# Kernel tuning notes

Hardware: AMD Instinct MI355X
Metric: run time of the kernel (lower is better)

Reference implementation:

```python
import jax, jax.numpy as jnp
import numpy as np

WINDOW = (2, 8, 8)  # (T, H, W); N = 128
NUM_HEADS = 6
DIM = 192


def _relative_position_index(ws):
    """NxN int index into the relative-position-bias table (faithful port)."""
    d, h, w = np.meshgrid(np.arange(ws[0]), np.arange(ws[1]), np.arange(ws[2]), indexing='ij')
    coords = np.stack([d, h, w]).reshape(3, -1)            # (3, N)
    rel = coords[:, :, None] - coords[:, None, :]          # (3, N, N)
    rel = rel.transpose(1, 2, 0).astype(np.int64)          # (N, N, 3)
    rel[:, :, 0] += ws[0] - 1
    rel[:, :, 1] += ws[1] - 1
    rel[:, :, 2] += ws[2] - 1
    rel[:, :, 0] *= (2 * ws[1] - 1) * (2 * ws[2] - 1)
    rel[:, :, 1] *= 2 * ws[2] - 1
    return rel.sum(-1)                                     # (N, N)


def setup_inputs() -> dict:
    key = jax.random.key(0)
    k1, k2, k3, k4, k5, k6 = jax.random.split(key, 6)
    N = WINDOW[0] * WINDOW[1] * WINDOW[2]                  # 128
    B_ = 1024                                              # num_windows * batch
    nW = 64
    table_len = (2 * WINDOW[0] - 1) * (2 * WINDOW[1] - 1) * (2 * WINDOW[2] - 1)  # 675
    x = jax.random.normal(k1, (B_, N, DIM), dtype=jnp.float32)
    mask = jax.random.normal(k2, (nW, N, N), dtype=jnp.float32)  # additive attn mask
    qkv_w = jax.random.normal(k3, (3 * DIM, DIM), dtype=jnp.float32) * 0.02
    proj_w = jax.random.normal(k4, (DIM, DIM), dtype=jnp.float32) * 0.02
    proj_b = jax.random.normal(k5, (DIM,), dtype=jnp.float32) * 0.02
    rpb_table = jax.random.normal(k6, (table_len, NUM_HEADS), dtype=jnp.float32) * 0.02
    rel_index = jnp.asarray(_relative_position_index(WINDOW), dtype=jnp.int32)
    return {"x": x, "mask": mask, "qkv_w": qkv_w, "proj_w": proj_w,
            "proj_b": proj_b, "rpb_table": rpb_table, "rel_index": rel_index}


def reference(x, mask, qkv_w, proj_w, proj_b, rpb_table, rel_index):
    B_, N, C = x.shape
    H = NUM_HEADS
    hd = C // H
    scale = hd ** (-0.5)
    # qkv projection (no bias, qkv_bias=False)
    qkv = (x @ qkv_w.T).reshape(B_, N, 3, H, hd)
    q, k, v = qkv[:, :, 0], qkv[:, :, 1], qkv[:, :, 2]      # (B_, N, H, hd)
    # windowed attention scores
    attn = jnp.einsum('bnhd,bmhd->bhnm', q * scale, k)      # (B_, H, N, N)
    # gathered relative-position bias: (N, N, H) -> (H, N, N)
    bias = rpb_table[rel_index.reshape(-1)].reshape(N, N, H).transpose(2, 0, 1)
    attn = attn + bias[None]
    # shift-window mask: (nW, N, N) broadcast over batch groups and heads
    nW = mask.shape[0]
    attn = attn.reshape(B_ // nW, nW, H, N, N) + mask[None, :, None]
    attn = attn.reshape(B_, H, N, N)
    attn = jax.nn.softmax(attn, axis=-1)
    out = jnp.einsum('bhnm,bmhd->bnhd', attn, v).reshape(B_, N, C)
    return out @ proj_w.T + proj_b
```

## Files before the change

### kernel.cpp

```cpp
#include <hip/hip_runtime.h>
#include <hip/hip_bf16.h>


typedef float f32x4 __attribute__((ext_vector_type(4)));
typedef short short8 __attribute__((ext_vector_type(8)));
typedef short short4e __attribute__((ext_vector_type(4)));

#define SCALE 0.17677669529663687f
#define LOG2E 1.4426950408889634f

static __device__ __forceinline__ short f2bf(float f) {
  __hip_bfloat16 h = __float2bfloat16(f);
  return __builtin_bit_cast(short, h);
}
static __device__ __forceinline__ f32x4 mfma16(short8 a, short8 b, f32x4 c) {
  return __builtin_amdgcn_mfma_f32_16x16x32_bf16(a, b, c, 0, 0, 0);
}

__global__ __launch_bounds__(256) void prep_w(const float* __restrict__ qkvw,
                                              const float* __restrict__ projw,
                                              short* __restrict__ wbf,
                                              short* __restrict__ pwbf) {
  int t = blockIdx.x * 256 + threadIdx.x;
  const int NQ = 27648;
  float4 f; short* dst;
  if (t < NQ) { f = ((const float4*)qkvw)[t]; dst = wbf + t * 4; }
  else        { f = ((const float4*)projw)[t - NQ]; dst = pwbf + (t - NQ) * 4; }
  short4e o; o[0] = f2bf(f.x); o[1] = f2bf(f.y); o[2] = f2bf(f.z); o[3] = f2bf(f.w);
  *(short4e*)dst = o;
}

__global__ __launch_bounds__(256) void prep_bias(const int* __restrict__ rel,
                                                 const float* __restrict__ table,
                                                 float* __restrict__ biasF) {
  int blk = blockIdx.x;
  int h = blk >> 4, L = blk & 15;
  int tid = threadIdx.x, lane = tid & 63, wave = tid >> 6;
  int lr = lane & 15, r4 = (lane >> 4) * 4;
  int rf = L >> 3, rg = (L >> 1) & 3, cp = L & 1;
  int row = wave * 32 + rf * 16 + r4 + rg;
  float4 v;
#pragma unroll
  for (int e = 0; e < 4; ++e) {
    int col = (cp * 4 + e) * 16 + lr;
    ((float*)&v)[e] = table[rel[row * 128 + col] * 6 + h] * LOG2E;
  }
  ((float4*)(biasF + (size_t)h * 16384))[L * 256 + tid] = v;
}

__global__ __launch_bounds__(256) void prep_mask(const float* __restrict__ mask,
                                                 float* __restrict__ maskF) {
  int blk = blockIdx.x;
  int w = blk >> 4, L = blk & 15;
  int tid = threadIdx.x, lane = tid & 63, wave = tid >> 6;
  int lr = lane & 15, r4 = (lane >> 4) * 4;
  int rf = L >> 3, rg = (L >> 1) & 3, cp = L & 1;
  int row = wave * 32 + rf * 16 + r4 + rg;
  const float* src = mask + (size_t)w * 16384 + row * 128;
  float4 v;
#pragma unroll
  for (int e = 0; e < 4; ++e) {
    int col = (cp * 4 + e) * 16 + lr;
    ((float*)&v)[e] = src[col] * LOG2E;
  }
  ((float4*)(maskF + (size_t)w * 16384))[L * 256 + tid] = v;
}

__global__ __launch_bounds__(256, 2) void qkv_kernel(const float* __restrict__ x,
                                                     const short* __restrict__ wbf,
                                                     short* __restrict__ qb,
                                                     short* __restrict__ kb,
                                                     short* __restrict__ vb) {
  __shared__ short xt[24576];
  __shared__ short wt[2][6144];
  const int b = blockIdx.x, tid = threadIdx.x;
  const int wave = tid >> 6, lane = tid & 63;
  const int lr = lane & 15, g = lane >> 4;
  const int g16 = g * 16, r4 = g * 4;
  const int rowbase = wave * 32;
  const int xorkey = (lr & 7) << 4;
  char* xtb = (char*)xt;
  char* wtb = (char*)wt;

  int wsoff[3], wdoff[3];
#pragma unroll
  for (int i = 0; i < 3; ++i) {
    int idx8 = i * 256 + tid;
    int r = idx8 / 24, c = idx8 - r * 24;
    wsoff[i] = idx8 * 8;
    wdoff[i] = r * 384 + ((c * 16) ^ ((r & 7) << 4));
  }
  short8 wreg[3];
#pragma unroll
  for (int i = 0; i < 3; ++i) wreg[i] = *(const short8*)(wbf + wsoff[i]);

  const float4* xr = (const float4*)(x + (size_t)b * 24576);
  for (int s = tid; s < 6144; s += 256) {
    float4 f = xr[s];
    int r = s / 48, c8 = s - r * 48;
    int off = r * 384 + ((c8 * 8) ^ ((r & 7) << 4));
    short4e o; o[0] = f2bf(f.x); o[1] = f2bf(f.y); o[2] = f2bf(f.z); o[3] = f2bf(f.w);
    *(short4e*)(xtb + off) = o;
  }
#pragma unroll
  for (int i = 0; i < 3; ++i) *(short8*)(wtb + wdoff[i]) = wreg[i];
  __syncthreads();

  const int rA0 = (rowbase + lr) * 384, rA1 = rA0 + 16 * 384;
  const int wB0 = lr * 384, wB1 = wB0 + 16 * 384;

  for (int ch = 0; ch < 18; ++ch) {
    if (ch < 17) {
#pragma unroll
      for (int i = 0; i < 3; ++i)
        wreg[i] = *(const short8*)(wbf + (ch + 1) * 6144 + wsoff[i]);
    }
    const char* wbuf = wtb + (ch & 1) * 12288;
    f32x4 acc[2][2];
    acc[0][0] = acc[0][1] = acc[1][0] = acc[1][1] = f32x4{0.f, 0.f, 0.f, 0.f};
    const bool isv = (ch >= 12);
#pragma unroll
    for (int ks = 0; ks < 6; ++ks) {
      int cx = (ks * 64 + g16) ^ xorkey;
      short8 xa0 = *(const short8*)(xtb + rA0 + cx);
      short8 xa1 = *(const short8*)(xtb + rA1 + cx);
      short8 wf0 = *(const short8*)(wbuf + wB0 + cx);
      short8 wf1 = *(const short8*)(wbuf + wB1 + cx);
      if (!isv) {
        acc[0][0] = mfma16(xa0, wf0, acc[0][0]);
        acc[0][1] = mfma16(xa0, wf1, acc[0][1]);
        acc[1][0] = mfma16(xa1, wf0, acc[1][0]);
        acc[1][1] = mfma16(xa1, wf1, acc[1][1]);
      } else {
        acc[0][0] = mfma16(wf0, xa0, acc[0][0]);
        acc[0][1] = mfma16(wf0, xa1, acc[0][1]);
        acc[1][0] = mfma16(wf1, xa0, acc[1][0]);
        acc[1][1] = mfma16(wf1, xa1, acc[1][1]);
      }
    }
    if (!isv) {
      int h = (ch < 6) ? ch : ch - 6;
      short* dst = (ch < 6) ? qb : kb;
      float sc = (ch < 6) ? (SCALE * LOG2E) : 1.0f;
      size_t base = ((size_t)b * 6 + h) * 4096;
#pragma unroll
      for (int rf = 0; rf < 2; ++rf)
#pragma unroll
        for (int cf = 0; cf < 2; ++cf) {
          int d = cf * 16 + lr;
#pragma unroll
          for (int rg = 0; rg < 4; ++rg) {
            int tok = rowbase + rf * 16 + r4 + rg;
            dst[base + (size_t)tok * 32 + d] = f2bf(acc[rf][cf][rg] * sc);
          }
        }
    } else {
      int h = ch - 12;
      size_t base = ((size_t)b * 6 + h) * 4096;
#pragma unroll
      for (int jf = 0; jf < 2; ++jf)
#pragma unroll
        for (int tf = 0; tf < 2; ++tf) {
          int tok = rowbase + tf * 16 + lr;
#pragma unroll
          for (int rg = 0; rg < 4; ++rg) {
            int d = jf * 16 + r4 + rg;
            vb[base + (size_t)d * 128 + tok] = f2bf(acc[jf][tf][rg]);
          }
        }
    }
    if (ch < 17) {
#pragma unroll
      for (int i = 0; i < 3; ++i)
        *(short8*)(wtb + ((ch + 1) & 1) * 12288 + wdoff[i]) = wreg[i];
      __syncthreads();
    }
  }
}

template <bool BF16OUT>
__global__ __launch_bounds__(256, 4) void attn_kernel(const short* __restrict__ qb,
                                                      const short* __restrict__ kb,
                                                      const short* __restrict__ vb,
                                                      const float* __restrict__ biasF,
                                                      const float* __restrict__ maskF,
                                                      float* __restrict__ aoutf,
                                                      short* __restrict__ aoutb) {
  __shared__ short p_lds[16384];
  char* pbuf = (char*)p_lds;
  const int bh = blockIdx.x, b = bh / 6, h = bh - b * 6;
  const short* qt = qb + (size_t)bh * 4096;
  const short* kt = kb + (size_t)bh * 4096;
  const short* vt = vb + (size_t)bh * 4096;
  const float4* bF4 = (const float4*)(biasF + (size_t)h * 16384);
  const float4* mF4 = (const float4*)(maskF + (size_t)(b & 63) * 16384);
  const int tid = threadIdx.x, wave = tid >> 6, lane = tid & 63;
  const int lr = lane & 15, g = lane >> 4, lkb = g * 8, r4 = g * 4;
  const int rowbase = wave * 32;

  float inv[2][4];
#pragma unroll
  for (int rf = 0; rf < 2; ++rf) {
    short8 a0 = *(const short8*)&qt[(rowbase + rf * 16 + lr) * 32 + lkb];
    f32x4 s[8];
    __builtin_amdgcn_s_setprio(1);
#pragma unroll
    for (int cf = 0; cf < 8; ++cf) {
      short8 bb = *(const short8*)&kt[(cf * 16 + lr) * 32 + lkb];
      f32x4 z = {0.f, 0.f, 0.f, 0.f};
      s[cf] = mfma16(a0, bb, z);
    }
    __builtin_amdgcn_s_setprio(0);
#pragma unroll
    for (int rg = 0; rg < 4; ++rg) {
      int L = rf * 8 + rg * 2;
      float4 bb0 = bF4[L * 256 + tid];
      float4 bb1 = bF4[(L + 1) * 256 + tid];
      float4 mm0 = mF4[L * 256 + tid];
      float4 mm1 = mF4[(L + 1) * 256 + tid];
      float p0 = exp2f(s[0][rg] + bb0.x + mm0.x);
      float p1 = exp2f(s[1][rg] + bb0.y + mm0.y);
      float p2 = exp2f(s[2][rg] + bb0.z + mm0.z);
      float p3 = exp2f(s[3][rg] + bb0.w + mm0.w);
      float p4 = exp2f(s[4][rg] + bb1.x + mm1.x);
      float p5 = exp2f(s[5][rg] + bb1.y + mm1.y);
      float p6 = exp2f(s[6][rg] + bb1.z + mm1.z);
      float p7 = exp2f(s[7][rg] + bb1.w + mm1.w);
      float sum = ((p0 + p1) + (p2 + p3)) + ((p4 + p5) + (p6 + p7));
#pragma unroll
      for (int o = 1; o < 16; o <<= 1) sum += __shfl_xor(sum, o);
      inv[rf][rg] = 1.0f / sum;
      int row = rowbase + rf * 16 + r4 + rg;
      int base = (row << 8) + (lr << 1);
      int swz = (row & 15) << 4;
      *(short*)(pbuf + ((base + 0 * 32) ^ swz)) = f2bf(p0);
      *(short*)(pbuf + ((base + 1 * 32) ^ swz)) = f2bf(p1);
      *(short*)(pbuf + ((base + 2 * 32) ^ swz)) = f2bf(p2);
      *(short*)(pbuf + ((base + 3 * 32) ^ swz)) = f2bf(p3);
      *(short*)(pbuf + ((base + 4 * 32) ^ swz)) = f2bf(p4);
      *(short*)(pbuf + ((base + 5 * 32) ^ swz)) = f2bf(p5);
      *(short*)(pbuf + ((base + 6 * 32) ^ swz)) = f2bf(p6);
      *(short*)(pbuf + ((base + 7 * 32) ^ swz)) = f2bf(p7);
    }
  }
  const int rsw = lr << 4;
  f32x4 o[2][2];
  o[0][0] = o[0][1] = o[1][0] = o[1][1] = f32x4{0.f, 0.f, 0.f, 0.f};
#pragma unroll
  for (int ks = 0; ks < 4; ++ks) {
    int ra = ((rowbase + lr) << 8) + (ks << 6) + (g << 4);
    short8 pa0 = *(const short8*)(pbuf + ((ra) ^ rsw));
    short8 pa1 = *(const short8*)(pbuf + ((ra + (16 << 8)) ^ rsw));
    short8 b0 = *(const short8*)&vt[lr * 128 + ks * 32 + lkb];
    short8 b1 = *(const short8*)&vt[(16 + lr) * 128 + ks * 32 + lkb];
    __builtin_amdgcn_s_setprio(1);
    o[0][0] = mfma16(pa0, b0, o[0][0]);
    o[0][1] = mfma16(pa0, b1, o[0][1]);
    o[1][0] = mfma16(pa1, b0, o[1][0]);
    o[1][1] = mfma16(pa1, b1, o[1][1]);
    __builtin_amdgcn_s_setprio(0);
  }
#pragma unroll
  for (int rf = 0; rf < 2; ++rf)
#pragma unroll
    for (int cf = 0; cf < 2; ++cf)
#pragma unroll
      for (int rg = 0; rg < 4; ++rg) {
        int tok = rowbase + rf * 16 + r4 + rg;
        int d = cf * 16 + lr;
        float val = o[rf][cf][rg] * inv[rf][rg];
        if constexpr (BF16OUT)
          aoutb[((size_t)b * 128 + tok) * 192 + h * 32 + d] = f2bf(val);
        else
          aoutf[((size_t)b * 128 + tok) * 192 + h * 32 + d] = val;
      }
}

template <bool BF16IN>
__global__ __launch_bounds__(256, 2) void proj_kernel(const float* __restrict__ ainf,
                                                      const short* __restrict__ ainb,
                                                      const short* __restrict__ pwbf,
                                                      const float* __restrict__ pb,
                                                      float* __restrict__ out) {
  __shared__ short at[24576];
  __shared__ short wt[2][6144];
  const int b = blockIdx.x, tid = threadIdx.x;
  const int wave = tid >> 6, lane = tid & 63;
  const int lr = lane & 15, g = lane >> 4;
  const int g16 = g * 16, r4 = g * 4;
  const int rowbase = wave * 32;
  const int xorkey = (lr & 7) << 4;
  char* atb = (char*)at;
  char* wtb = (char*)wt;

  int wsoff[3], wdoff[3];
#pragma unroll
  for (int i = 0; i < 3; ++i) {
    int idx8 = i * 256 + tid;
    int r = idx8 / 24, c = idx8 - r * 24;
    wsoff[i] = idx8 * 8;
    wdoff[i] = r * 384 + ((c * 16) ^ ((r & 7) << 4));
  }
  short8 wreg[3];
#pragma unroll
  for (int i = 0; i < 3; ++i) wreg[i] = *(const short8*)(pwbf + wsoff[i]);

  if constexpr (BF16IN) {
    const short8* ar = (const short8*)(ainb + (size_t)b * 24576);
#pragma unroll
    for (int i = 0; i < 12; ++i) {
      int idx8 = i * 256 + tid;
      int r = idx8 / 24, c = idx8 - r * 24;
      short8 v = ar[idx8];
      *(short8*)(atb + r * 384 + ((c * 16) ^ ((r & 7) << 4))) = v;
    }
  } else {
    const float4* ar = (const float4*)(ainf + (size_t)b * 24576);
    for (int s = tid; s < 6144; s += 256) {
      float4 f = ar[s];
      int r = s / 48, c8 = s - r * 48;
      int off = r * 384 + ((c8 * 8) ^ ((r & 7) << 4));
      short4e o; o[0] = f2bf(f.x); o[1] = f2bf(f.y); o[2] = f2bf(f.z); o[3] = f2bf(f.w);
      *(short4e*)(atb + off) = o;
    }
  }
#pragma unroll
  for (int i = 0; i < 3; ++i) *(short8*)(wtb + wdoff[i]) = wreg[i];
  __syncthreads();

  const int rA0 = (rowbase + lr) * 384, rA1 = rA0 + 16 * 384;
  const int wB0 = lr * 384, wB1 = wB0 + 16 * 384;

  for (int ch = 0; ch < 6; ++ch) {
    if (ch < 5) {
#pragma unroll
      for (int i = 0; i < 3; ++i)
        wreg[i] = *(const short8*)(pwbf + (ch + 1) * 6144 + wsoff[i]);
    }
    const char* wbuf = wtb + (ch & 1) * 12288;
    f32x4 acc[2][2];
    acc[0][0] = acc[0][1] = acc[1][0] = acc[1][1] = f32x4{0.f, 0.f, 0.f, 0.f};
#pragma unroll
    for (int ks = 0; ks < 6; ++ks) {
      int cx = (ks * 64 + g16) ^ xorkey;
      short8 xa0 = *(const short8*)(atb + rA0 + cx);
      short8 xa1 = *(const short8*)(atb + rA1 + cx);
      short8 wf0 = *(const short8*)(wbuf + wB0 + cx);
      short8 wf1 = *(const short8*)(wbuf + wB1 + cx);
      acc[0][0] = mfma16(xa0, wf0, acc[0][0]);
      acc[0][1] = mfma16(xa0, wf1, acc[0][1]);
      acc[1][0] = mfma16(xa1, wf0, acc[1][0]);
      acc[1][1] = mfma16(xa1, wf1, acc[1][1]);
    }
#pragma unroll
    for (int cf = 0; cf < 2; ++cf) {
      int j = ch * 32 + cf * 16 + lr;
      float bj = pb[j];
#pragma unroll
      for (int rf = 0; rf < 2; ++rf)
#pragma unroll
        for (int rg = 0; rg < 4; ++rg) {
          int tok = rowbase + rf * 16 + r4 + rg;
          out[((size_t)b * 128 + tok) * 192 + j] = acc[rf][cf][rg] + bj;
        }
    }
    if (ch < 5) {
#pragma unroll
      for (int i = 0; i < 3; ++i)
        *(short8*)(wtb + ((ch + 1) & 1) * 12288 + wdoff[i]) = wreg[i];
      __syncthreads();
    }
  }
}

extern "C" void kernel_launch(void* const* d_in, const int* in_sizes, int n_in,
                              void* d_out, int out_size, void* d_ws, size_t ws_size,
                              hipStream_t stream) {
  const float* x      = (const float*)d_in[0];
  const float* mask   = (const float*)d_in[1];
  const float* qkv_w  = (const float*)d_in[2];
  const float* proj_w = (const float*)d_in[3];
  const float* proj_b = (const float*)d_in[4];
  const float* table  = (const float*)d_in[5];
  const int*   rel    = (const int*)d_in[6];
  char* ws = (char*)d_ws;
  size_t o = 0;
  float* biasF = (float*)(ws + o); o += 393216;
  float* maskF = (float*)(ws + o); o += 4194304;
  short* wbf   = (short*)(ws + o); o += 221184;
  short* pwbf  = (short*)(ws + o); o += 73728;
  short* qbp   = (short*)(ws + o); o += 50331648;
  short* kbp   = (short*)(ws + o); o += 50331648;
  short* vbp   = (short*)(ws + o); o += 50331648;
  bool bf16path = (ws_size >= o + 50331648);
  short* aoutb = (short*)(ws + o);
  float* out = (float*)d_out;

  prep_w<<<144, 256, 0, stream>>>(qkv_w, proj_w, wbf, pwbf);
  prep_bias<<<96, 256, 0, stream>>>(rel, table, biasF);
  prep_mask<<<1024, 256, 0, stream>>>(mask, maskF);
  qkv_kernel<<<1024, 256, 0, stream>>>(x, wbf, qbp, kbp, vbp);
  if (bf16path) {
    attn_kernel<true><<<6144, 256, 0, stream>>>(qbp, kbp, vbp, biasF, maskF, nullptr, aoutb);
    proj_kernel<true><<<1024, 256, 0, stream>>>(nullptr, aoutb, pwbf, proj_b, out);
  } else {
    attn_kernel<false><<<6144, 256, 0, stream>>>(qbp, kbp, vbp, biasF, maskF, out, nullptr);
    proj_kernel<false><<<1024, 256, 0, stream>>>(out, nullptr, pwbf, proj_b, out);
  }
}
```

Before: 199.2 us.

## Fuse QKV projection and attention into one per-window kernel

```diff
diff --git a/kernel.cpp b/kernel.cpp
--- a/kernel.cpp
+++ b/kernel.cpp
@@ -8,6 +8,7 @@
 
 #define SCALE 0.17677669529663687f
 #define LOG2E 1.4426950408889634f
+#define QSC (SCALE * LOG2E)
 
 static __device__ __forceinline__ short f2bf(float f) {
   __hip_bfloat16 h = __float2bfloat16(f);
@@ -66,219 +67,187 @@
   ((float4*)(maskF + (size_t)w * 16384))[L * 256 + tid] = v;
 }
 
-__global__ __launch_bounds__(256, 2) void qkv_kernel(const float* __restrict__ x,
-                                                     const short* __restrict__ wbf,
-                                                     short* __restrict__ qb,
-                                                     short* __restrict__ kb,
-                                                     short* __restrict__ vb) {
-  __shared__ short xt[24576];
-  __shared__ short wt[2][6144];
-  const int b = blockIdx.x, tid = threadIdx.x;
-  const int wave = tid >> 6, lane = tid & 63;
-  const int lr = lane & 15, g = lane >> 4;
-  const int g16 = g * 16, r4 = g * 4;
+__global__ __launch_bounds__(256, 2) void fused_kernel(const float* __restrict__ x,
+                                                       const short* __restrict__ wbf,
+                                                       const float* __restrict__ biasF,
+                                                       const float* __restrict__ maskF,
+                                                       short* __restrict__ aoutb) {
+  __shared__ short q_lds[128 * 40];
+  __shared__ short k_lds[128 * 40];
+  __shared__ short v_lds[32 * 136];
+  __shared__ short p_lds[128 * 128];
+  char* pbuf = (char*)p_lds;
+  const char* vbuf = (const char*)v_lds;
+  const int b = blockIdx.x;
+  const int tid = threadIdx.x, wave = tid >> 6, lane = tid & 63;
+  const int lr = lane & 15, g = lane >> 4, r4 = g * 4;
   const int rowbase = wave * 32;
-  const int xorkey = (lr & 7) << 4;
-  char* xtb = (char*)xt;
-  char* wtb = (char*)wt;
-
-  int wsoff[3], wdoff[3];
-#pragma unroll
-  for (int i = 0; i < 3; ++i) {
-    int idx8 = i * 256 + tid;
-    int r = idx8 / 24, c = idx8 - r * 24;
-    wsoff[i] = idx8 * 8;
-    wdoff[i] = r * 384 + ((c * 16) ^ ((r & 7) << 4));
-  }
-  short8 wreg[3];
-#pragma unroll
-  for (int i = 0; i < 3; ++i) wreg[i] = *(const short8*)(wbf + wsoff[i]);
-
-  const float4* xr = (const float4*)(x + (size_t)b * 24576);
-  for (int s = tid; s < 6144; s += 256) {
-    float4 f = xr[s];
-    int r = s / 48, c8 = s - r * 48;
-    int off = r * 384 + ((c8 * 8) ^ ((r & 7) << 4));
-    short4e o; o[0] = f2bf(f.x); o[1] = f2bf(f.y); o[2] = f2bf(f.z); o[3] = f2bf(f.w);
-    *(short4e*)(xtb + off) = o;
-  }
-#pragma unroll
-  for (int i = 0; i < 3; ++i) *(short8*)(wtb + wdoff[i]) = wreg[i];
-  __syncthreads();
-
-  const int rA0 = (rowbase + lr) * 384, rA1 = rA0 + 16 * 384;
-  const int wB0 = lr * 384, wB1 = wB0 + 16 * 384;
-
-  for (int ch = 0; ch < 18; ++ch) {
-    if (ch < 17) {
-#pragma unroll
-      for (int i = 0; i < 3; ++i)
-        wreg[i] = *(const short8*)(wbf + (ch + 1) * 6144 + wsoff[i]);
-    }
-    const char* wbuf = wtb + (ch & 1) * 12288;
-    f32x4 acc[2][2];
-    acc[0][0] = acc[0][1] = acc[1][0] = acc[1][1] = f32x4{0.f, 0.f, 0.f, 0.f};
-    const bool isv = (ch >= 12);
-#pragma unroll
-    for (int ks = 0; ks < 6; ++ks) {
-      int cx = (ks * 64 + g16) ^ xorkey;
-      short8 xa0 = *(const short8*)(xtb + rA0 + cx);
-      short8 xa1 = *(const short8*)(xtb + rA1 + cx);
-      short8 wf0 = *(const short8*)(wbuf + wB0 + cx);
-      short8 wf1 = *(const short8*)(wbuf + wB1 + cx);
-      if (!isv) {
-        acc[0][0] = mfma16(xa0, wf0, acc[0][0]);
-        acc[0][1] = mfma16(xa0, wf1, acc[0][1]);
-        acc[1][0] = mfma16(xa1, wf0, acc[1][0]);
-        acc[1][1] = mfma16(xa1, wf1, acc[1][1]);
-      } else {
-        acc[0][0] = mfma16(wf0, xa0, acc[0][0]);
-        acc[0][1] = mfma16(wf0, xa1, acc[0][1]);
-        acc[1][0] = mfma16(wf1, xa0, acc[1][0]);
-        acc[1][1] = mfma16(wf1, xa1, acc[1][1]);
-      }
-    }
-    if (!isv) {
-      int h = (ch < 6) ? ch : ch - 6;
-      short* dst = (ch < 6) ? qb : kb;
-      float sc = (ch < 6) ? (SCALE * LOG2E) : 1.0f;
-      size_t base = ((size_t)b * 6 + h) * 4096;
+  const float4* mF4 = (const float4*)(maskF + (size_t)(b & 63) * 16384);
+
+  short8 xa[2][6];
+  {
+    const float* xr = x + (size_t)b * 24576 + (size_t)(rowbase + lr) * 192;
+#pragma unroll
+    for (int rf = 0; rf < 2; ++rf)
+#pragma unroll
+      for (int ks = 0; ks < 6; ++ks) {
+        const float* p = xr + rf * 16 * 192 + ks * 32 + g * 8;
+        float4 f0 = *(const float4*)p;
+        float4 f1 = *(const float4*)(p + 4);
+        short8 v8;
+        v8[0] = f2bf(f0.x); v8[1] = f2bf(f0.y); v8[2] = f2bf(f0.z); v8[3] = f2bf(f0.w);
+        v8[4] = f2bf(f1.x); v8[5] = f2bf(f1.y); v8[6] = f2bf(f1.z); v8[7] = f2bf(f1.w);
+        xa[rf][ks] = v8;
+      }
+  }
+
+  for (int h = 0; h < 6; ++h) {
+    {
+      f32x4 a[2][2];
+      a[0][0] = a[0][1] = a[1][0] = a[1][1] = f32x4{0.f, 0.f, 0.f, 0.f};
+#pragma unroll
+      for (int cf = 0; cf < 2; ++cf) {
+        const short* wr = wbf + (size_t)(h * 32 + cf * 16 + lr) * 192 + g * 8;
+#pragma unroll
+        for (int ks = 0; ks < 6; ++ks) {
+          short8 wf = *(const short8*)(wr + ks * 32);
+          a[0][cf] = mfma16(xa[0][ks], wf, a[0][cf]);
+          a[1][cf] = mfma16(xa[1][ks], wf, a[1][cf]);
+        }
+      }
 #pragma unroll
       for (int rf = 0; rf < 2; ++rf)
 #pragma unroll
-        for (int cf = 0; cf < 2; ++cf) {
-          int d = cf * 16 + lr;
-#pragma unroll
-          for (int rg = 0; rg < 4; ++rg) {
-            int tok = rowbase + rf * 16 + r4 + rg;
-            dst[base + (size_t)tok * 32 + d] = f2bf(acc[rf][cf][rg] * sc);
-          }
+        for (int cf = 0; cf < 2; ++cf)
+#pragma unroll
+          for (int rg = 0; rg < 4; ++rg)
+            q_lds[(rowbase + rf * 16 + r4 + rg) * 40 + cf * 16 + lr] =
+                f2bf(a[rf][cf][rg] * QSC);
+    }
+    {
+      f32x4 a[2][2];
+      a[0][0] = a[0][1] = a[1][0] = a[1][1] = f32x4{0.f, 0.f, 0.f, 0.f};
+#pragma unroll
+      for (int cf = 0; cf < 2; ++cf) {
+        const short* wr = wbf + (size_t)(192 + h * 32 + cf * 16 + lr) * 192 + g * 8;
+#pragma unroll
+        for (int ks = 0; ks < 6; ++ks) {
+          short8 wf = *(const short8*)(wr + ks * 32);
+          a[0][cf] = mfma16(xa[0][ks], wf, a[0][cf]);
+          a[1][cf] = mfma16(xa[1][ks], wf, a[1][cf]);
         }
-    } else {
-      int h = ch - 12;
-      size_t base = ((size_t)b * 6 + h) * 4096;
-#pragma unroll
-      for (int jf = 0; jf < 2; ++jf)
-#pragma unroll
-        for (int tf = 0; tf < 2; ++tf) {
-          int tok = rowbase + tf * 16 + lr;
-#pragma unroll
-          for (int rg = 0; rg < 4; ++rg) {
-            int d = jf * 16 + r4 + rg;
-            vb[base + (size_t)d * 128 + tok] = f2bf(acc[jf][tf][rg]);
-          }
+      }
+#pragma unroll
+      for (int rf = 0; rf < 2; ++rf)
+#pragma unroll
+        for (int cf = 0; cf < 2; ++cf)
+#pragma unroll
+          for (int rg = 0; rg < 4; ++rg)
+            k_lds[(rowbase + rf * 16 + r4 + rg) * 40 + cf * 16 + lr] =
+                f2bf(a[rf][cf][rg]);
+    }
+    {
+      f32x4 a[2][2];
+      a[0][0] = a[0][1] = a[1][0] = a[1][1] = f32x4{0.f, 0.f, 0.f, 0.f};
+#pragma unroll
+      for (int df = 0; df < 2; ++df) {
+        const short* wr = wbf + (size_t)(384 + h * 32 + df * 16 + lr) * 192 + g * 8;
+#pragma unroll
+        for (int ks = 0; ks < 6; ++ks) {
+          short8 wf = *(const short8*)(wr + ks * 32);
+          a[df][0] = mfma16(wf, xa[0][ks], a[df][0]);
+          a[df][1] = mfma16(wf, xa[1][ks], a[df][1]);
         }
-    }
-    if (ch < 17) {
-#pragma unroll
-      for (int i = 0; i < 3; ++i)
-        *(short8*)(wtb + ((ch + 1) & 1) * 12288 + wdoff[i]) = wreg[i];
-      __syncthreads();
-    }
-  }
-}
-
-template <bool BF16OUT>
-__global__ __launch_bounds__(256, 4) void attn_kernel(const short* __restrict__ qb,
-                                                      const short* __restrict__ kb,
-                                                      const short* __restrict__ vb,
-                                                      const float* __restrict__ biasF,
-                                                      const float* __restrict__ maskF,
-                                                      float* __restrict__ aoutf,
-                                                      short* __restrict__ aoutb) {
-  __shared__ short p_lds[16384];
-  char* pbuf = (char*)p_lds;
-  const int bh = blockIdx.x, b = bh / 6, h = bh - b * 6;
-  const short* qt = qb + (size_t)bh * 4096;
-  const short* kt = kb + (size_t)bh * 4096;
-  const short* vt = vb + (size_t)bh * 4096;
-  const float4* bF4 = (const float4*)(biasF + (size_t)h * 16384);
-  const float4* mF4 = (const float4*)(maskF + (size_t)(b & 63) * 16384);
-  const int tid = threadIdx.x, wave = tid >> 6, lane = tid & 63;
-  const int lr = lane & 15, g = lane >> 4, lkb = g * 8, r4 = g * 4;
-  const int rowbase = wave * 32;
-
-  float inv[2][4];
-#pragma unroll
-  for (int rf = 0; rf < 2; ++rf) {
-    short8 a0 = *(const short8*)&qt[(rowbase + rf * 16 + lr) * 32 + lkb];
-    f32x4 s[8];
-    __builtin_amdgcn_s_setprio(1);
-#pragma unroll
-    for (int cf = 0; cf < 8; ++cf) {
-      short8 bb = *(const short8*)&kt[(cf * 16 + lr) * 32 + lkb];
-      f32x4 z = {0.f, 0.f, 0.f, 0.f};
-      s[cf] = mfma16(a0, bb, z);
-    }
-    __builtin_amdgcn_s_setprio(0);
-#pragma unroll
-    for (int rg = 0; rg < 4; ++rg) {
-      int L = rf * 8 + rg * 2;
-      float4 bb0 = bF4[L * 256 + tid];
-      float4 bb1 = bF4[(L + 1) * 256 + tid];
-      float4 mm0 = mF4[L * 256 + tid];
-      float4 mm1 = mF4[(L + 1) * 256 + tid];
-      float p0 = exp2f(s[0][rg] + bb0.x + mm0.x);
-      float p1 = exp2f(s[1][rg] + bb0.y + mm0.y);
-      float p2 = exp2f(s[2][rg] + bb0.z + mm0.z);
-      float p3 = exp2f(s[3][rg] + bb0.w + mm0.w);
-      float p4 = exp2f(s[4][rg] + bb1.x + mm1.x);
-      float p5 = exp2f(s[5][rg] + bb1.y + mm1.y);
-      float p6 = exp2f(s[6][rg] + bb1.z + mm1.z);
-      float p7 = exp2f(s[7][rg] + bb1.w + mm1.w);
-      float sum = ((p0 + p1) + (p2 + p3)) + ((p4 + p5) + (p6 + p7));
-#pragma unroll
-      for (int o = 1; o < 16; o <<= 1) sum += __shfl_xor(sum, o);
-      inv[rf][rg] = 1.0f / sum;
-      int row = rowbase + rf * 16 + r4 + rg;
-      int base = (row << 8) + (lr << 1);
-      int swz = (row & 15) << 4;
-      *(short*)(pbuf + ((base + 0 * 32) ^ swz)) = f2bf(p0);
-      *(short*)(pbuf + ((base + 1 * 32) ^ swz)) = f2bf(p1);
-      *(short*)(pbuf + ((base + 2 * 32) ^ swz)) = f2bf(p2);
-      *(short*)(pbuf + ((base + 3 * 32) ^ swz)) = f2bf(p3);
-      *(short*)(pbuf + ((base + 4 * 32) ^ swz)) = f2bf(p4);
-      *(short*)(pbuf + ((base + 5 * 32) ^ swz)) = f2bf(p5);
-      *(short*)(pbuf + ((base + 6 * 32) ^ swz)) = f2bf(p6);
-      *(short*)(pbuf + ((base + 7 * 32) ^ swz)) = f2bf(p7);
-    }
-  }
-  const int rsw = lr << 4;
-  f32x4 o[2][2];
-  o[0][0] = o[0][1] = o[1][0] = o[1][1] = f32x4{0.f, 0.f, 0.f, 0.f};
-#pragma unroll
-  for (int ks = 0; ks < 4; ++ks) {
-    int ra = ((rowbase + lr) << 8) + (ks << 6) + (g << 4);
-    short8 pa0 = *(const short8*)(pbuf + ((ra) ^ rsw));
-    short8 pa1 = *(const short8*)(pbuf + ((ra + (16 << 8)) ^ rsw));
-    short8 b0 = *(const short8*)&vt[lr * 128 + ks * 32 + lkb];
-    short8 b1 = *(const short8*)&vt[(16 + lr) * 128 + ks * 32 + lkb];
-    __builtin_amdgcn_s_setprio(1);
-    o[0][0] = mfma16(pa0, b0, o[0][0]);
-    o[0][1] = mfma16(pa0, b1, o[0][1]);
-    o[1][0] = mfma16(pa1, b0, o[1][0]);
-    o[1][1] = mfma16(pa1, b1, o[1][1]);
-    __builtin_amdgcn_s_setprio(0);
-  }
-#pragma unroll
-  for (int rf = 0; rf < 2; ++rf)
-#pragma unroll
-    for (int cf = 0; cf < 2; ++cf)
+      }
+#pragma unroll
+      for (int df = 0; df < 2; ++df)
+#pragma unroll
+        for (int tf = 0; tf < 2; ++tf)
+#pragma unroll
+          for (int rg = 0; rg < 4; ++rg)
+            v_lds[(df * 16 + r4 + rg) * 136 + rowbase + tf * 16 + lr] =
+                f2bf(a[df][tf][rg]);
+    }
+    __syncthreads();
+
+    const float4* bF4 = (const float4*)(biasF + (size_t)h * 16384);
+#pragma unroll
+    for (int rf = 0; rf < 2; ++rf) {
+      short8 qa = *(const short8*)(q_lds + (rowbase + rf * 16 + lr) * 40 + g * 8);
+      f32x4 s[8];
+      __builtin_amdgcn_s_setprio(1);
+#pragma unroll
+      for (int cf = 0; cf < 8; ++cf) {
+        short8 kb = *(const short8*)(k_lds + (cf * 16 + lr) * 40 + g * 8);
+        f32x4 z = {0.f, 0.f, 0.f, 0.f};
+        s[cf] = mfma16(qa, kb, z);
+      }
+      __builtin_amdgcn_s_setprio(0);
 #pragma unroll
       for (int rg = 0; rg < 4; ++rg) {
-        int tok = rowbase + rf * 16 + r4 + rg;
-        int d = cf * 16 + lr;
-        float val = o[rf][cf][rg] * inv[rf][rg];
-        if constexpr (BF16OUT)
-          aoutb[((size_t)b * 128 + tok) * 192 + h * 32 + d] = f2bf(val);
-        else
-          aoutf[((size_t)b * 128 + tok) * 192 + h * 32 + d] = val;
-      }
-}
-
-template <bool BF16IN>
-__global__ __launch_bounds__(256, 2) void proj_kernel(const float* __restrict__ ainf,
-                                                      const short* __restrict__ ainb,
+        int L = rf * 8 + rg * 2;
+        float4 bb0 = bF4[L * 256 + tid];
+        float4 bb1 = bF4[(L + 1) * 256 + tid];
+        float4 mm0 = mF4[L * 256 + tid];
+        float4 mm1 = mF4[(L + 1) * 256 + tid];
+        float p0 = exp2f(s[0][rg] + bb0.x + mm0.x);
+        float p1 = exp2f(s[1][rg] + bb0.y + mm0.y);
+        float p2 = exp2f(s[2][rg] + bb0.z + mm0.z);
+        float p3 = exp2f(s[3][rg] + bb0.w + mm0.w);
+        float p4 = exp2f(s[4][rg] + bb1.x + mm1.x);
+        float p5 = exp2f(s[5][rg] + bb1.y + mm1.y);
+        float p6 = exp2f(s[6][rg] + bb1.z + mm1.z);
+        float p7 = exp2f(s[7][rg] + bb1.w + mm1.w);
+        float sum = ((p0 + p1) + (p2 + p3)) + ((p4 + p5) + (p6 + p7));
+#pragma unroll
+        for (int o = 1; o < 16; o <<= 1) sum += __shfl_xor(sum, o);
+        float inv = 1.0f / sum;
+        int row = rowbase + rf * 16 + r4 + rg;
+        int base = (row << 8) + (lr << 1);
+        int swz = (row & 15) << 4;
+        *(short*)(pbuf + ((base + 0 * 32) ^ swz)) = f2bf(p0 * inv);
+        *(short*)(pbuf + ((base + 1 * 32) ^ swz)) = f2bf(p1 * inv);
+        *(short*)(pbuf + ((base + 2 * 32) ^ swz)) = f2bf(p2 * inv);
+        *(short*)(pbuf + ((base + 3 * 32) ^ swz)) = f2bf(p3 * inv);
+        *(short*)(pbuf + ((base + 4 * 32) ^ swz)) = f2bf(p4 * inv);
+        *(short*)(pbuf + ((base + 5 * 32) ^ swz)) = f2bf(p5 * inv);
+        *(short*)(pbuf + ((base + 6 * 32) ^ swz)) = f2bf(p6 * inv);
+        *(short*)(pbuf + ((base + 7 * 32) ^ swz)) = f2bf(p7 * inv);
+      }
+    }
+    f32x4 o_[2][2];
+    o_[0][0] = o_[0][1] = o_[1][0] = o_[1][1] = f32x4{0.f, 0.f, 0.f, 0.f};
+    const int rsw = lr << 4;
+#pragma unroll
+    for (int ks = 0; ks < 4; ++ks) {
+      short8 va0 = *(const short8*)(vbuf + lr * 272 + ks * 64 + g * 16);
+      short8 va1 = *(const short8*)(vbuf + (16 + lr) * 272 + ks * 64 + g * 16);
+      short8 pb0 = *(const short8*)(pbuf + ((((rowbase + lr) << 8) + (ks << 6) + (g << 4)) ^ rsw));
+      short8 pb1 = *(const short8*)(pbuf + ((((rowbase + 16 + lr) << 8) + (ks << 6) + (g << 4)) ^ rsw));
+      __builtin_amdgcn_s_setprio(1);
+      o_[0][0] = mfma16(va0, pb0, o_[0][0]);
+      o_[0][1] = mfma16(va0, pb1, o_[0][1]);
+      o_[1][0] = mfma16(va1, pb0, o_[1][0]);
+      o_[1][1] = mfma16(va1, pb1, o_[1][1]);
+      __builtin_amdgcn_s_setprio(0);
+    }
+#pragma unroll
+    for (int df = 0; df < 2; ++df)
+#pragma unroll
+      for (int tf = 0; tf < 2; ++tf) {
+        short4e s4;
+        s4[0] = f2bf(o_[df][tf][0]);
+        s4[1] = f2bf(o_[df][tf][1]);
+        s4[2] = f2bf(o_[df][tf][2]);
+        s4[3] = f2bf(o_[df][tf][3]);
+        *(short4e*)(aoutb + ((size_t)b * 128 + rowbase + tf * 16 + lr) * 192 +
+                    h * 32 + df * 16 + r4) = s4;
+      }
+    __syncthreads();
+  }
+}
+
+__global__ __launch_bounds__(256, 2) void proj_kernel(const short* __restrict__ ainb,
                                                       const short* __restrict__ pwbf,
                                                       const float* __restrict__ pb,
                                                       float* __restrict__ out) {
@@ -305,24 +274,13 @@
 #pragma unroll
   for (int i = 0; i < 3; ++i) wreg[i] = *(const short8*)(pwbf + wsoff[i]);
 
-  if constexpr (BF16IN) {
-    const short8* ar = (const short8*)(ainb + (size_t)b * 24576);
-#pragma unroll
-    for (int i = 0; i < 12; ++i) {
-      int idx8 = i * 256 + tid;
-      int r = idx8 / 24, c = idx8 - r * 24;
-      short8 v = ar[idx8];
-      *(short8*)(atb + r * 384 + ((c * 16) ^ ((r & 7) << 4))) = v;
-    }
-  } else {
-    const float4* ar = (const float4*)(ainf + (size_t)b * 24576);
-    for (int s = tid; s < 6144; s += 256) {
-      float4 f = ar[s];
-      int r = s / 48, c8 = s - r * 48;
-      int off = r * 384 + ((c8 * 8) ^ ((r & 7) << 4));
-      short4e o; o[0] = f2bf(f.x); o[1] = f2bf(f.y); o[2] = f2bf(f.z); o[3] = f2bf(f.w);
-      *(short4e*)(atb + off) = o;
-    }
+  const short8* ar = (const short8*)(ainb + (size_t)b * 24576);
+#pragma unroll
+  for (int i = 0; i < 12; ++i) {
+    int idx8 = i * 256 + tid;
+    int r = idx8 / 24, c = idx8 - r * 24;
+    short8 v = ar[idx8];
+    *(short8*)(atb + r * 384 + ((c * 16) ^ ((r & 7) << 4))) = v;
   }
 #pragma unroll
   for (int i = 0; i < 3; ++i) *(short8*)(wtb + wdoff[i]) = wreg[i];
@@ -389,22 +347,12 @@
   float* maskF = (float*)(ws + o); o += 4194304;
   short* wbf   = (short*)(ws + o); o += 221184;
   short* pwbf  = (short*)(ws + o); o += 73728;
-  short* qbp   = (short*)(ws + o); o += 50331648;
-  short* kbp   = (short*)(ws + o); o += 50331648;
-  short* vbp   = (short*)(ws + o); o += 50331648;
-  bool bf16path = (ws_size >= o + 50331648);
   short* aoutb = (short*)(ws + o);
   float* out = (float*)d_out;
 
   prep_w<<<144, 256, 0, stream>>>(qkv_w, proj_w, wbf, pwbf);
   prep_bias<<<96, 256, 0, stream>>>(rel, table, biasF);
   prep_mask<<<1024, 256, 0, stream>>>(mask, maskF);
-  qkv_kernel<<<1024, 256, 0, stream>>>(x, wbf, qbp, kbp, vbp);
-  if (bf16path) {
-    attn_kernel<true><<<6144, 256, 0, stream>>>(qbp, kbp, vbp, biasF, maskF, nullptr, aoutb);
-    proj_kernel<true><<<1024, 256, 0, stream>>>(nullptr, aoutb, pwbf, proj_b, out);
-  } else {
-    attn_kernel<false><<<6144, 256, 0, stream>>>(qbp, kbp, vbp, biasF, maskF, out, nullptr);
-    proj_kernel<false><<<1024, 256, 0, stream>>>(out, nullptr, pwbf, proj_b, out);
-  }
-}
+  fused_kernel<<<1024, 256, 0, stream>>>(x, wbf, biasF, maskF, aoutb);
+  proj_kernel<<<1024, 256, 0, stream>>>(aoutb, pwbf, proj_b, out);
+}
```

After: 235.8 us. 1.18x slower.

## Fuse bias and mask into one table and stage bf16 attention output in output buffer

Applied to the files above, without the earlier changes.

```diff
diff --git a/kernel.cpp b/kernel.cpp
--- a/kernel.cpp
+++ b/kernel.cpp
@@ -8,6 +8,7 @@
 
 #define SCALE 0.17677669529663687f
 #define LOG2E 1.4426950408889634f
+#define QSC (SCALE * LOG2E)
 
 static __device__ __forceinline__ short f2bf(float f) {
   __hip_bfloat16 h = __float2bfloat16(f);
@@ -30,40 +31,29 @@
   *(short4e*)dst = o;
 }
 
-__global__ __launch_bounds__(256) void prep_bias(const int* __restrict__ rel,
-                                                 const float* __restrict__ table,
-                                                 float* __restrict__ biasF) {
+__global__ __launch_bounds__(256) void prep_bm(const int* __restrict__ rel,
+                                               const float* __restrict__ table,
+                                               const float* __restrict__ mask,
+                                               float* __restrict__ bmF) {
   int blk = blockIdx.x;
-  int h = blk >> 4, L = blk & 15;
+  int h = blk >> 6, w = blk & 63;
   int tid = threadIdx.x, lane = tid & 63, wave = tid >> 6;
   int lr = lane & 15, r4 = (lane >> 4) * 4;
-  int rf = L >> 3, rg = (L >> 1) & 3, cp = L & 1;
-  int row = wave * 32 + rf * 16 + r4 + rg;
-  float4 v;
-#pragma unroll
-  for (int e = 0; e < 4; ++e) {
-    int col = (cp * 4 + e) * 16 + lr;
-    ((float*)&v)[e] = table[rel[row * 128 + col] * 6 + h] * LOG2E;
-  }
-  ((float4*)(biasF + (size_t)h * 16384))[L * 256 + tid] = v;
-}
-
-__global__ __launch_bounds__(256) void prep_mask(const float* __restrict__ mask,
-                                                 float* __restrict__ maskF) {
-  int blk = blockIdx.x;
-  int w = blk >> 4, L = blk & 15;
-  int tid = threadIdx.x, lane = tid & 63, wave = tid >> 6;
-  int lr = lane & 15, r4 = (lane >> 4) * 4;
-  int rf = L >> 3, rg = (L >> 1) & 3, cp = L & 1;
-  int row = wave * 32 + rf * 16 + r4 + rg;
-  const float* src = mask + (size_t)w * 16384 + row * 128;
-  float4 v;
-#pragma unroll
-  for (int e = 0; e < 4; ++e) {
-    int col = (cp * 4 + e) * 16 + lr;
-    ((float*)&v)[e] = src[col] * LOG2E;
-  }
-  ((float4*)(maskF + (size_t)w * 16384))[L * 256 + tid] = v;
+  const float* mk = mask + (size_t)w * 16384;
+  float* dst = bmF + (size_t)blk * 16384;
+#pragma unroll
+  for (int L = 0; L < 16; ++L) {
+    int rf = L >> 3, rg = (L >> 1) & 3, cp = L & 1;
+    int row = wave * 32 + rf * 16 + r4 + rg;
+    float4 v;
+#pragma unroll
+    for (int e = 0; e < 4; ++e) {
+      int col = (cp * 4 + e) * 16 + lr;
+      float bias = table[rel[row * 128 + col] * 6 + h];
+      ((float*)&v)[e] = (bias + mk[row * 128 + col]) * LOG2E;
+    }
+    ((float4*)dst)[L * 256 + tid] = v;
+  }
 }
 
 __global__ __launch_bounds__(256, 2) void qkv_kernel(const float* __restrict__ x,
@@ -141,7 +131,7 @@
     if (!isv) {
       int h = (ch < 6) ? ch : ch - 6;
       short* dst = (ch < 6) ? qb : kb;
-      float sc = (ch < 6) ? (SCALE * LOG2E) : 1.0f;
+      float sc = (ch < 6) ? QSC : 1.0f;
       size_t base = ((size_t)b * 6 + h) * 4096;
 #pragma unroll
       for (int rf = 0; rf < 2; ++rf)
@@ -178,22 +168,19 @@
   }
 }
 
-template <bool BF16OUT>
-__global__ __launch_bounds__(256, 4) void attn_kernel(const short* __restrict__ qb,
+__global__ __launch_bounds__(256, 5) void attn_kernel(const short* __restrict__ qb,
                                                       const short* __restrict__ kb,
                                                       const short* __restrict__ vb,
-                                                      const float* __restrict__ biasF,
-                                                      const float* __restrict__ maskF,
-                                                      float* __restrict__ aoutf,
-                                                      short* __restrict__ aoutb) {
+                                                      const float* __restrict__ bmF,
+                                                      char* __restrict__ outc) {
   __shared__ short p_lds[16384];
   char* pbuf = (char*)p_lds;
   const int bh = blockIdx.x, b = bh / 6, h = bh - b * 6;
   const short* qt = qb + (size_t)bh * 4096;
   const short* kt = kb + (size_t)bh * 4096;
   const short* vt = vb + (size_t)bh * 4096;
-  const float4* bF4 = (const float4*)(biasF + (size_t)h * 16384);
-  const float4* mF4 = (const float4*)(maskF + (size_t)(b & 63) * 16384);
+  const float4* bm4 = (const float4*)(bmF + ((size_t)h * 64 + (b & 63)) * 16384);
+  short* outSlot = (short*)(outc + (size_t)b * 98304 + 49152);
   const int tid = threadIdx.x, wave = tid >> 6, lane = tid & 63;
   const int lr = lane & 15, g = lane >> 4, lkb = g * 8, r4 = g * 4;
   const int rowbase = wave * 32;
@@ -214,18 +201,16 @@
 #pragma unroll
     for (int rg = 0; rg < 4; ++rg) {
       int L = rf * 8 + rg * 2;
-      float4 bb0 = bF4[L * 256 + tid];
-      float4 bb1 = bF4[(L + 1) * 256 + tid];
-      float4 mm0 = mF4[L * 256 + tid];
-      float4 mm1 = mF4[(L + 1) * 256 + tid];
-      float p0 = exp2f(s[0][rg] + bb0.x + mm0.x);
-      float p1 = exp2f(s[1][rg] + bb0.y + mm0.y);
-      float p2 = exp2f(s[2][rg] + bb0.z + mm0.z);
-      float p3 = exp2f(s[3][rg] + bb0.w + mm0.w);
-      float p4 = exp2f(s[4][rg] + bb1.x + mm1.x);
-      float p5 = exp2f(s[5][rg] + bb1.y + mm1.y);
-      float p6 = exp2f(s[6][rg] + bb1.z + mm1.z);
-      float p7 = exp2f(s[7][rg] + bb1.w + mm1.w);
+      float4 bb0 = bm4[L * 256 + tid];
+      float4 bb1 = bm4[(L + 1) * 256 + tid];
+      float p0 = exp2f(s[0][rg] + bb0.x);
+      float p1 = exp2f(s[1][rg] + bb0.y);
+      float p2 = exp2f(s[2][rg] + bb0.z);
+      float p3 = exp2f(s[3][rg] + bb0.w);
+      float p4 = exp2f(s[4][rg] + bb1.x);
+      float p5 = exp2f(s[5][rg] + bb1.y);
+      float p6 = exp2f(s[6][rg] + bb1.z);
+      float p7 = exp2f(s[7][rg] + bb1.w);
       float sum = ((p0 + p1) + (p2 + p3)) + ((p4 + p5) + (p6 + p7));
 #pragma unroll
       for (int o = 1; o < 16; o <<= 1) sum += __shfl_xor(sum, o);
@@ -268,18 +253,11 @@
       for (int rg = 0; rg < 4; ++rg) {
         int tok = rowbase + rf * 16 + r4 + rg;
         int d = cf * 16 + lr;
-        float val = o[rf][cf][rg] * inv[rf][rg];
-        if constexpr (BF16OUT)
-          aoutb[((size_t)b * 128 + tok) * 192 + h * 32 + d] = f2bf(val);
-        else
-          aoutf[((size_t)b * 128 + tok) * 192 + h * 32 + d] = val;
+        outSlot[tok * 192 + h * 32 + d] = f2bf(o[rf][cf][rg] * inv[rf][rg]);
       }
 }
 
-template <bool BF16IN>
-__global__ __launch_bounds__(256, 2) void proj_kernel(const float* __restrict__ ainf,
-                                                      const short* __restrict__ ainb,
-                                                      const short* __restrict__ pwbf,
+__global__ __launch_bounds__(256, 2) void proj_kernel(const short* __restrict__ pwbf,
                                                       const float* __restrict__ pb,
                                                       float* __restrict__ out) {
   __shared__ short at[24576];
@@ -305,24 +283,13 @@
 #pragma unroll
   for (int i = 0; i < 3; ++i) wreg[i] = *(const short8*)(pwbf + wsoff[i]);
 
-  if constexpr (BF16IN) {
-    const short8* ar = (const short8*)(ainb + (size_t)b * 24576);
-#pragma unroll
-    for (int i = 0; i < 12; ++i) {
-      int idx8 = i * 256 + tid;
-      int r = idx8 / 24, c = idx8 - r * 24;
-      short8 v = ar[idx8];
-      *(short8*)(atb + r * 384 + ((c * 16) ^ ((r & 7) << 4))) = v;
-    }
-  } else {
-    const float4* ar = (const float4*)(ainf + (size_t)b * 24576);
-    for (int s = tid; s < 6144; s += 256) {
-      float4 f = ar[s];
-      int r = s / 48, c8 = s - r * 48;
-      int off = r * 384 + ((c8 * 8) ^ ((r & 7) << 4));
-      short4e o; o[0] = f2bf(f.x); o[1] = f2bf(f.y); o[2] = f2bf(f.z); o[3] = f2bf(f.w);
-      *(short4e*)(atb + off) = o;
-    }
+  const short8* ar = (const short8*)((const char*)out + (size_t)b * 98304 + 49152);
+#pragma unroll
+  for (int i = 0; i < 12; ++i) {
+    int idx8 = i * 256 + tid;
+    int r = idx8 / 24, c = idx8 - r * 24;
+    short8 v = ar[idx8];
+    *(short8*)(atb + r * 384 + ((c * 16) ^ ((r & 7) << 4))) = v;
   }
 #pragma unroll
   for (int i = 0; i < 3; ++i) *(short8*)(wtb + wdoff[i]) = wreg[i];
@@ -385,26 +352,17 @@
   const int*   rel    = (const int*)d_in[6];
   char* ws = (char*)d_ws;
   size_t o = 0;
-  float* biasF = (float*)(ws + o); o += 393216;
-  float* maskF = (float*)(ws + o); o += 4194304;
-  short* wbf   = (short*)(ws + o); o += 221184;
-  short* pwbf  = (short*)(ws + o); o += 73728;
-  short* qbp   = (short*)(ws + o); o += 50331648;
-  short* kbp   = (short*)(ws + o); o += 50331648;
-  short* vbp   = (short*)(ws + o); o += 50331648;
-  bool bf16path = (ws_size >= o + 50331648);
-  short* aoutb = (short*)(ws + o);
+  float* bmF  = (float*)(ws + o); o += 25165824;
+  short* wbf  = (short*)(ws + o); o += 221184;
+  short* pwbf = (short*)(ws + o); o += 73728;
+  short* qbp  = (short*)(ws + o); o += 50331648;
+  short* kbp  = (short*)(ws + o); o += 50331648;
+  short* vbp  = (short*)(ws + o); o += 50331648;
   float* out = (float*)d_out;
 
   prep_w<<<144, 256, 0, stream>>>(qkv_w, proj_w, wbf, pwbf);
-  prep_bias<<<96, 256, 0, stream>>>(rel, table, biasF);
-  prep_mask<<<1024, 256, 0, stream>>>(mask, maskF);
+  prep_bm<<<384, 256, 0, stream>>>(rel, table, mask, bmF);
   qkv_kernel<<<1024, 256, 0, stream>>>(x, wbf, qbp, kbp, vbp);
-  if (bf16path) {
-    attn_kernel<true><<<6144, 256, 0, stream>>>(qbp, kbp, vbp, biasF, maskF, nullptr, aoutb);
-    proj_kernel<true><<<1024, 256, 0, stream>>>(nullptr, aoutb, pwbf, proj_b, out);
-  } else {
-    attn_kernel<false><<<6144, 256, 0, stream>>>(qbp, kbp, vbp, biasF, maskF, out, nullptr);
-    proj_kernel<false><<<1024, 256, 0, stream>>>(out, nullptr, pwbf, proj_b, out);
-  }
-}
+  attn_kernel<<<6144, 256, 0, stream>>>(qbp, kbp, vbp, bmF, (char*)d_out);
+  proj_kernel<<<1024, 256, 0, stream>>>(pwbf, proj_b, out);
+}
```

New measurement: 201.7 us. Within noise of the previous version (+1.2%).
